# Optimization experiments

Measured on AMD Instinct MI355X. Metric: run time of the kernel, lower is better.

Reference implementation:

```python
import jax, jax.numpy as jnp
import numpy as np

B, T, I, H = 64, 512, 1024, 2048


def setup_inputs() -> dict:
    key = jax.random.key(0)
    ks = jax.random.split(key, 6)
    s = 1.0 / np.sqrt(H).astype(np.float32)
    return {
        "input": jax.random.normal(ks[0], (B, T, I), jnp.float32),
        "internal": jax.random.normal(ks[1], (B, T), jnp.float32) * 0.1,
        "w_ih": jax.random.uniform(ks[2], (H, I), jnp.float32, -s, s),
        "w_hh": jax.random.uniform(ks[3], (H, H), jnp.float32, -s, s),
        "b_ih": jax.random.uniform(ks[4], (H,), jnp.float32, -s, s),
        "b_hh": jax.random.uniform(ks[5], (H,), jnp.float32, -s, s),
        "h0": jnp.zeros((1, B, H), jnp.float32),
        "trunc": 64,
    }


def reference(input, internal, w_ih, w_hh, b_ih, b_hh, h0, trunc):
    # input: [B, T, I]; internal: [B, T] scalar-per-step drive; h0: [1, B, H]
    Tlen = input.shape[1]
    # Hoist the input projection out of the recurrence (same math, one big GEMM).
    x_proj = jnp.einsum('bti,hi->bth', input, w_ih) + b_ih  # [B, T, H]
    # Truncated-BPTT boundaries: state is detached when i % trunc == 0.
    detach_mask = (jnp.arange(Tlen) % trunc) == 0  # [T] bool

    def step(h, xs):
        xp, noise, m = xs  # xp: [B, H], noise: [B], m: scalar bool
        # detach state at truncation boundary (no-op in forward pass)
        h = jnp.where(m, jax.lax.stop_gradient(h), h)
        h_new = jnp.tanh(xp + noise[:, None] + h @ w_hh.T + b_hh)
        return h_new, h_new

    h_last, outs = jax.lax.scan(
        step, h0[0], (x_proj.transpose(1, 0, 2), internal.T, detach_mask))
    # outputs: [B, T, H], final state: [1, B, H]
    return outs.transpose(1, 0, 2), h_last[None]
```

## Files before the change

kernel.cpp:

```cpp
#include <hip/hip_runtime.h>
#include <hip/hip_bf16.h>
#include <math.h>

#define Bb 64
#define Tt 512
#define Ii 1024
#define Hh 2048
#define NBLK 128

typedef __attribute__((ext_vector_type(8))) short bf16x8;
typedef __attribute__((ext_vector_type(8))) unsigned short ushort8;
typedef __attribute__((ext_vector_type(4))) float f32x4;

__device__ __forceinline__ unsigned short f2bf(float x) {
    unsigned int u = __float_as_uint(x);
    unsigned int r = u + 0x7fffu + ((u >> 16) & 1u);
    return (unsigned short)(r >> 16);
}

__global__ __launch_bounds__(256) void cvt_kernel(
    const float* __restrict__ src, unsigned short* __restrict__ dst)
{
    const int i = (blockIdx.x * 256 + threadIdx.x) * 4;
    float4 v = *(const float4*)(src + i);
    ushort4 o;
    o.x = f2bf(v.x); o.y = f2bf(v.y); o.z = f2bf(v.z); o.w = f2bf(v.w);
    *(ushort4*)(dst + i) = o;
}

__global__ __launch_bounds__(512) void init_flags(unsigned int* flags) {
    flags[threadIdx.x] = 0u;
}

__global__ __launch_bounds__(256, 2) void xproj_kernel(
    const float* __restrict__ A,
    const unsigned short* __restrict__ Wbf,
    const float* __restrict__ bias,
    float* __restrict__ out)
{
    __shared__ unsigned short As[128 * 40];
    __shared__ unsigned short Bs[128 * 40];

    const int tid  = threadIdx.x;
    const int lane = tid & 63;
    const int wid  = tid >> 6;
    const int wm   = wid & 1;
    const int wn   = wid >> 1;
    const int rlo  = lane & 15;
    const int khi  = lane >> 4;

    const int m0 = blockIdx.y * 128;
    const int n0 = blockIdx.x * 128;

    f32x4 acc[4][4];
    #pragma unroll
    for (int i = 0; i < 4; ++i)
        #pragma unroll
        for (int j = 0; j < 4; ++j) acc[i][j] = (f32x4)0.f;

    for (int k0 = 0; k0 < Ii; k0 += 32) {
        #pragma unroll
        for (int p = 0; p < 4; ++p) {
            const int flat = p * 256 + tid;
            const int row  = flat >> 3;
            const int c4   = flat & 7;
            float4 v = *(const float4*)(A + (size_t)(m0 + row) * Ii + k0 + c4 * 4);
            ushort4 o;
            o.x = f2bf(v.x); o.y = f2bf(v.y); o.z = f2bf(v.z); o.w = f2bf(v.w);
            *(ushort4*)(As + row * 40 + c4 * 4) = o;
        }
        #pragma unroll
        for (int p = 0; p < 2; ++p) {
            const int flat = p * 256 + tid;
            const int row  = flat >> 2;
            const int c8   = flat & 3;
            ushort8 v = *(const ushort8*)(Wbf + (size_t)(n0 + row) * Ii + k0 + c8 * 8);
            *(ushort8*)(Bs + row * 40 + c8 * 8) = v;
        }
        __syncthreads();

        bf16x8 af[4], bfr[4];
        #pragma unroll
        for (int i = 0; i < 4; ++i)
            af[i] = *(const bf16x8*)(As + (wm * 64 + i * 16 + rlo) * 40 + khi * 8);
        #pragma unroll
        for (int j = 0; j < 4; ++j)
            bfr[j] = *(const bf16x8*)(Bs + (wn * 64 + j * 16 + rlo) * 40 + khi * 8);
        #pragma unroll
        for (int i = 0; i < 4; ++i)
            #pragma unroll
            for (int j = 0; j < 4; ++j)
                acc[i][j] = __builtin_amdgcn_mfma_f32_16x16x32_bf16(
                    af[i], bfr[j], acc[i][j], 0, 0, 0);
        __syncthreads();
    }

    #pragma unroll
    for (int j = 0; j < 4; ++j) {
        const int col = n0 + wn * 64 + j * 16 + rlo;
        const float bj = bias[col];
        #pragma unroll
        for (int i = 0; i < 4; ++i) {
            #pragma unroll
            for (int r = 0; r < 4; ++r) {
                const int m = m0 + wm * 64 + i * 16 + khi * 4 + r;
                out[(size_t)m * Hh + col] = acc[i][j][r] + bj;
            }
        }
    }
}

#define LD_FRAG(dst, base, OFF)                                               \
    asm volatile("global_load_dwordx4 %0, %1, off offset:" OFF " sc0 sc1"     \
                 : "=v"(dst) : "v"(base))

#define LD_FRAG_C(dst, base, OFF)                                             \
    asm volatile("global_load_dwordx4 %0, %1, off offset:" OFF                \
                 : "=v"(dst) : "v"(base))

#define DRAIN16(a)                                                            \
    asm volatile("s_waitcnt vmcnt(0)"                                         \
                 : "+v"(a[0][0]), "+v"(a[0][1]), "+v"(a[0][2]), "+v"(a[0][3]),\
                   "+v"(a[0][4]), "+v"(a[0][5]), "+v"(a[0][6]), "+v"(a[0][7]),\
                   "+v"(a[1][0]), "+v"(a[1][1]), "+v"(a[1][2]), "+v"(a[1][3]),\
                   "+v"(a[1][4]), "+v"(a[1][5]), "+v"(a[1][6]), "+v"(a[1][7]) \
                 :: "memory");                                                \
    __builtin_amdgcn_sched_barrier(0)

#define RAW_BARRIER()                                                         \
    asm volatile("s_waitcnt lgkmcnt(0)\n\ts_barrier" ::: "memory")

__global__ __launch_bounds__(512, 2) void rnn_persistent(
    const unsigned short* __restrict__ w_bf,
    unsigned short* __restrict__ h_bf,
    const float* __restrict__ b_hh,
    const float* __restrict__ internal,
    float* __restrict__ out,
    unsigned int* __restrict__ flags)
{
    __shared__ f32x4 red4[2][8 * 256];

    const int tid  = threadIdx.x;
    const int lane = tid & 63;
    const int wid  = tid >> 6;
    const int rlo  = lane & 15;
    const int khi  = lane >> 4;
    const int blk  = blockIdx.x;
    const int rh   = blk & 1;
    const int cg   = blk >> 1;

    bf16x8 wf[2][8];
    {
        const unsigned short* w0 =
            w_bf + (size_t)(cg * 32 + rlo) * Hh + wid * 256 + khi * 8;
        const unsigned short* w1 = w0 + (size_t)16 * Hh;
        LD_FRAG_C(wf[0][0], w0, "0");   LD_FRAG_C(wf[0][1], w0, "64");
        LD_FRAG_C(wf[0][2], w0, "128"); LD_FRAG_C(wf[0][3], w0, "192");
        LD_FRAG_C(wf[0][4], w0, "256"); LD_FRAG_C(wf[0][5], w0, "320");
        LD_FRAG_C(wf[0][6], w0, "384"); LD_FRAG_C(wf[0][7], w0, "448");
        LD_FRAG_C(wf[1][0], w1, "0");   LD_FRAG_C(wf[1][1], w1, "64");
        LD_FRAG_C(wf[1][2], w1, "128"); LD_FRAG_C(wf[1][3], w1, "192");
        LD_FRAG_C(wf[1][4], w1, "256"); LD_FRAG_C(wf[1][5], w1, "320");
        LD_FRAG_C(wf[1][6], w1, "384"); LD_FRAG_C(wf[1][7], w1, "448");
        DRAIN16(wf);
    }

    const int em    = (tid >> 6) & 1;
    const int ent   = (tid >> 7) & 1;
    const int odd   = lane & 1;
    const int clloc = (ent * 16 + rlo) & ~1;
    const int cl    = cg * 32 + clloc;
    const int rAl   = em * 16 + khi * 4 + 2 * odd;
    const int rAg   = rh * 32 + rAl;
    const int rBg   = rAg + 1;
    const float2 bh2 = (tid < 256) ? *(const float2*)(b_hh + cl)
                                   : make_float2(0.f, 0.f);

    float2 xpA = make_float2(0.f, 0.f), xpB = make_float2(0.f, 0.f);
    float  nzA = 0.f, nzB = 0.f;
    if (tid < 256) {
        xpA = *(const float2*)(out + ((size_t)rAg * Tt + 0) * Hh + cl);
        xpB = *(const float2*)(out + ((size_t)rBg * Tt + 0) * Hh + cl);
        nzA = internal[rAg * Tt + 0];
        nzB = internal[rBg * Tt + 0];
    }
    float2 gA_d = make_float2(0.f, 0.f), gB_d = make_float2(0.f, 0.f);

    unsigned int*       myflag = flags + rh * 256 + cg * 4 + wid;
    const unsigned int* pollf  = flags + rh * 256 + wid * 32 + (lane & 31);

    for (int t = 0; t < Tt; ++t) {
        const bool last = (t == Tt - 1);
        const unsigned short* h_cur = h_bf + (size_t)(t & 1) * Bb * Hh;
        unsigned short*       h_nxt = h_bf + (size_t)((t + 1) & 1) * Bb * Hh;

        if (t) {
            const unsigned int tgt = (unsigned int)t;
            while (true) {
                unsigned int f = __hip_atomic_load(
                    pollf, __ATOMIC_RELAXED, __HIP_MEMORY_SCOPE_AGENT);
                if (__all(f >= tgt)) break;
                __builtin_amdgcn_s_sleep(1);
            }
        }

        const unsigned short* am0 =
            h_cur + (size_t)(rh * 32 + rlo) * Hh + wid * 256 + khi * 8;
        const unsigned short* am1 = am0 + (size_t)16 * Hh;

        bf16x8 a[2][8];
        LD_FRAG(a[0][0], am0, "0");   LD_FRAG(a[0][1], am0, "64");
        LD_FRAG(a[0][2], am0, "128"); LD_FRAG(a[0][3], am0, "192");
        LD_FRAG(a[0][4], am0, "256"); LD_FRAG(a[0][5], am0, "320");
        LD_FRAG(a[0][6], am0, "384"); LD_FRAG(a[0][7], am0, "448");
        LD_FRAG(a[1][0], am1, "0");   LD_FRAG(a[1][1], am1, "64");
        LD_FRAG(a[1][2], am1, "128"); LD_FRAG(a[1][3], am1, "192");
        LD_FRAG(a[1][4], am1, "256"); LD_FRAG(a[1][5], am1, "320");
        LD_FRAG(a[1][6], am1, "384"); LD_FRAG(a[1][7], am1, "448");

        if (tid < 256 && t > 0) {
            *(float2*)(out + ((size_t)rAg * Tt + (t - 1)) * Hh + cl) = gA_d;
            *(float2*)(out + ((size_t)rBg * Tt + (t - 1)) * Hh + cl) = gB_d;
        }

        DRAIN16(a);

        f32x4 acc[2][2];
        #pragma unroll
        for (int m = 0; m < 2; ++m)
            #pragma unroll
            for (int nt = 0; nt < 2; ++nt) acc[m][nt] = (f32x4)0.f;
        #pragma unroll
        for (int kk = 0; kk < 8; ++kk)
            #pragma unroll
            for (int m = 0; m < 2; ++m)
                #pragma unroll
                for (int nt = 0; nt < 2; ++nt)
                    acc[m][nt] = __builtin_amdgcn_mfma_f32_16x16x32_bf16(
                        a[m][kk], wf[nt][kk], acc[m][nt], 0, 0, 0);

        f32x4* rb = red4[t & 1];
        #pragma unroll
        for (int nt = 0; nt < 2; ++nt)
            #pragma unroll
            for (int m = 0; m < 2; ++m)
                rb[wid * 256 + (nt * 2 + m) * 64 + lane] = acc[m][nt];
        RAW_BARRIER();

        if (tid < 256) {
            f32x4 s4 = (f32x4)0.f;
            #pragma unroll
            for (int ks = 0; ks < 8; ++ks)
                s4 += rb[ks * 256 + tid];

            f32x4 o4;
            #pragma unroll
            for (int i = 0; i < 4; ++i)
                o4[i] = __shfl_xor(s4[i], 1, 64);

            const float sA_lo = odd ? o4[2] : s4[0];
            const float sA_hi = odd ? s4[2] : o4[0];
            const float sB_lo = odd ? o4[3] : s4[1];
            const float sB_hi = odd ? s4[3] : o4[1];

            float2 gA, gB;
            gA.x = tanhf(xpA.x + nzA + bh2.x + sA_lo);
            gA.y = tanhf(xpA.y + nzA + bh2.y + sA_hi);
            gB.x = tanhf(xpB.x + nzB + bh2.x + sB_lo);
            gB.y = tanhf(xpB.y + nzB + bh2.y + sB_hi);

            const unsigned int hpA =
                (unsigned int)f2bf(gA.x) | ((unsigned int)f2bf(gA.y) << 16);
            const unsigned int hpB =
                (unsigned int)f2bf(gB.x) | ((unsigned int)f2bf(gB.y) << 16);
            __hip_atomic_store((unsigned int*)h_nxt + ((size_t)rAg * Hh + cl) / 2,
                               hpA, __ATOMIC_RELAXED, __HIP_MEMORY_SCOPE_AGENT);
            __hip_atomic_store((unsigned int*)h_nxt + ((size_t)rBg * Hh + cl) / 2,
                               hpB, __ATOMIC_RELAXED, __HIP_MEMORY_SCOPE_AGENT);

            if (last) {
                *(float2*)(out + ((size_t)rAg * Tt + t) * Hh + cl) = gA;
                *(float2*)(out + ((size_t)rBg * Tt + t) * Hh + cl) = gB;
                float* tail = out + (size_t)Bb * Tt * Hh;
                *(float2*)(tail + (size_t)rAg * Hh + cl) = gA;
                *(float2*)(tail + (size_t)rBg * Hh + cl) = gB;
            } else {
                gA_d = gA; gB_d = gB;

                asm volatile("s_waitcnt vmcnt(0)" ::: "memory");
                if (lane == 0)
                    __hip_atomic_store(myflag, (unsigned int)(t + 1),
                                       __ATOMIC_RELAXED,
                                       __HIP_MEMORY_SCOPE_AGENT);

                xpA = *(const float2*)(out + ((size_t)rAg * Tt + t + 1) * Hh + cl);
                xpB = *(const float2*)(out + ((size_t)rBg * Tt + t + 1) * Hh + cl);
                nzA = internal[rAg * Tt + t + 1];
                nzB = internal[rBg * Tt + t + 1];
            }
        }
    }
}

extern "C" void kernel_launch(void* const* d_in, const int* in_sizes, int n_in,
                              void* d_out, int out_size, void* d_ws, size_t ws_size,
                              hipStream_t stream) {
    const float* input    = (const float*)d_in[0];
    const float* internal = (const float*)d_in[1];
    const float* w_ih     = (const float*)d_in[2];
    const float* w_hh     = (const float*)d_in[3];
    const float* b_ih     = (const float*)d_in[4];
    const float* b_hh     = (const float*)d_in[5];
    const float* h0       = (const float*)d_in[6];
    float* out = (float*)d_out;

    unsigned short* w_hh_bf = (unsigned short*)d_ws;
    unsigned short* w_ih_bf = w_hh_bf + (size_t)Hh * Hh;
    unsigned short* h_bf    = w_ih_bf + (size_t)Hh * Ii;
    unsigned int*   flags   = (unsigned int*)(h_bf + (size_t)2 * Bb * Hh);

    hipLaunchKernelGGL(init_flags, dim3(1), dim3(512), 0, stream, flags);
    hipLaunchKernelGGL(cvt_kernel, dim3((Hh * Hh) / 1024), dim3(256), 0, stream,
                       w_hh, w_hh_bf);
    hipLaunchKernelGGL(cvt_kernel, dim3((Hh * Ii) / 1024), dim3(256), 0, stream,
                       w_ih, w_ih_bf);
    hipLaunchKernelGGL(cvt_kernel, dim3((Bb * Hh) / 1024), dim3(256), 0, stream,
                       h0, h_bf);

    dim3 g1(Hh / 128, (Bb * Tt) / 128);
    hipLaunchKernelGGL(xproj_kernel, g1, dim3(256), 0, stream,
                       input, w_ih_bf, b_ih, out);

    void* args[] = {(void*)&w_hh_bf, (void*)&h_bf, (void*)&b_hh,
                    (void*)&internal, (void*)&out, (void*)&flags};
    hipLaunchCooperativeKernel((void*)rnn_persistent, dim3(NBLK), dim3(512),
                               args, 0, stream);
}
```

Measured before the change: 4.002 ms.

## Halve persistent RNN grid and interleave two batch-half phases per block

```diff
diff --git a/kernel.cpp b/kernel.cpp
--- a/kernel.cpp
+++ b/kernel.cpp
@@ -6,7 +6,7 @@
 #define Tt 512
 #define Ii 1024
 #define Hh 2048
-#define NBLK 128
+#define NBLK 64
 
 typedef __attribute__((ext_vector_type(8))) short bf16x8;
 typedef __attribute__((ext_vector_type(8))) unsigned short ushort8;
@@ -26,6 +26,19 @@
     ushort4 o;
     o.x = f2bf(v.x); o.y = f2bf(v.y); o.z = f2bf(v.z); o.w = f2bf(v.w);
     *(ushort4*)(dst + i) = o;
+}
+
+__global__ __launch_bounds__(256) void cvt_h0(
+    const float* __restrict__ h0, unsigned short* __restrict__ hb)
+{
+    const int idx = (blockIdx.x * 256 + threadIdx.x) * 4;
+    const int b   = idx >> 11;
+    const int col = idx & 2047;
+    float4 v = *(const float4*)(h0 + idx);
+    ushort4 o;
+    o.x = f2bf(v.x); o.y = f2bf(v.y); o.z = f2bf(v.z); o.w = f2bf(v.w);
+    const int ph = b >> 5, r = b & 31;
+    *(ushort4*)(hb + (size_t)(ph * 64 + r) * Hh + col) = o;
 }
 
 __global__ __launch_bounds__(512) void init_flags(unsigned int* flags) {
@@ -145,9 +158,7 @@
     const int wid  = tid >> 6;
     const int rlo  = lane & 15;
     const int khi  = lane >> 4;
-    const int blk  = blockIdx.x;
-    const int rh   = blk & 1;
-    const int cg   = blk >> 1;
+    const int cg   = blockIdx.x;
 
     bf16x8 wf[2][8];
     {
@@ -171,132 +182,148 @@
     const int clloc = (ent * 16 + rlo) & ~1;
     const int cl    = cg * 32 + clloc;
     const int rAl   = em * 16 + khi * 4 + 2 * odd;
-    const int rAg   = rh * 32 + rAl;
-    const int rBg   = rAg + 1;
     const float2 bh2 = (tid < 256) ? *(const float2*)(b_hh + cl)
                                    : make_float2(0.f, 0.f);
 
-    float2 xpA = make_float2(0.f, 0.f), xpB = make_float2(0.f, 0.f);
-    float  nzA = 0.f, nzB = 0.f;
+    float2 xpA[2], xpB[2], gAd[2], gBd[2];
+    float  nzA[2], nzB[2];
+    #pragma unroll
+    for (int ph = 0; ph < 2; ++ph) {
+        xpA[ph] = make_float2(0.f, 0.f); xpB[ph] = make_float2(0.f, 0.f);
+        gAd[ph] = make_float2(0.f, 0.f); gBd[ph] = make_float2(0.f, 0.f);
+        nzA[ph] = 0.f; nzB[ph] = 0.f;
+    }
     if (tid < 256) {
-        xpA = *(const float2*)(out + ((size_t)rAg * Tt + 0) * Hh + cl);
-        xpB = *(const float2*)(out + ((size_t)rBg * Tt + 0) * Hh + cl);
-        nzA = internal[rAg * Tt + 0];
-        nzB = internal[rBg * Tt + 0];
-    }
-    float2 gA_d = make_float2(0.f, 0.f), gB_d = make_float2(0.f, 0.f);
-
-    unsigned int*       myflag = flags + rh * 256 + cg * 4 + wid;
-    const unsigned int* pollf  = flags + rh * 256 + wid * 32 + (lane & 31);
+        #pragma unroll
+        for (int ph = 0; ph < 2; ++ph) {
+            const int rA = ph * 32 + rAl, rB = rA + 1;
+            xpA[ph] = *(const float2*)(out + ((size_t)rA * Tt + 0) * Hh + cl);
+            xpB[ph] = *(const float2*)(out + ((size_t)rB * Tt + 0) * Hh + cl);
+            nzA[ph] = internal[rA * Tt + 0];
+            nzB[ph] = internal[rB * Tt + 0];
+        }
+    }
 
     for (int t = 0; t < Tt; ++t) {
         const bool last = (t == Tt - 1);
-        const unsigned short* h_cur = h_bf + (size_t)(t & 1) * Bb * Hh;
-        unsigned short*       h_nxt = h_bf + (size_t)((t + 1) & 1) * Bb * Hh;
-
-        if (t) {
-            const unsigned int tgt = (unsigned int)t;
-            while (true) {
-                unsigned int f = __hip_atomic_load(
-                    pollf, __ATOMIC_RELAXED, __HIP_MEMORY_SCOPE_AGENT);
-                if (__all(f >= tgt)) break;
-                __builtin_amdgcn_s_sleep(1);
+        #pragma unroll
+        for (int ph = 0; ph < 2; ++ph) {
+            const unsigned short* h_cur =
+                h_bf + (size_t)(ph * 64 + (t & 1) * 32) * Hh;
+            unsigned short* h_nxt =
+                h_bf + (size_t)(ph * 64 + ((t + 1) & 1) * 32) * Hh;
+
+            if (t) {
+                const unsigned int tgt = (unsigned int)t;
+                const unsigned int* pf =
+                    flags + ph * 256 + wid * 32 + (lane & 31);
+                while (true) {
+                    unsigned int f = __hip_atomic_load(
+                        pf, __ATOMIC_RELAXED, __HIP_MEMORY_SCOPE_AGENT);
+                    if (__all(f >= tgt)) break;
+                    __builtin_amdgcn_s_sleep(1);
+                }
             }
-        }
-
-        const unsigned short* am0 =
-            h_cur + (size_t)(rh * 32 + rlo) * Hh + wid * 256 + khi * 8;
-        const unsigned short* am1 = am0 + (size_t)16 * Hh;
-
-        bf16x8 a[2][8];
-        LD_FRAG(a[0][0], am0, "0");   LD_FRAG(a[0][1], am0, "64");
-        LD_FRAG(a[0][2], am0, "128"); LD_FRAG(a[0][3], am0, "192");
-        LD_FRAG(a[0][4], am0, "256"); LD_FRAG(a[0][5], am0, "320");
-        LD_FRAG(a[0][6], am0, "384"); LD_FRAG(a[0][7], am0, "448");
-        LD_FRAG(a[1][0], am1, "0");   LD_FRAG(a[1][1], am1, "64");
-        LD_FRAG(a[1][2], am1, "128"); LD_FRAG(a[1][3], am1, "192");
-        LD_FRAG(a[1][4], am1, "256"); LD_FRAG(a[1][5], am1, "320");
-        LD_FRAG(a[1][6], am1, "384"); LD_FRAG(a[1][7], am1, "448");
-
-        if (tid < 256 && t > 0) {
-            *(float2*)(out + ((size_t)rAg * Tt + (t - 1)) * Hh + cl) = gA_d;
-            *(float2*)(out + ((size_t)rBg * Tt + (t - 1)) * Hh + cl) = gB_d;
-        }
-
-        DRAIN16(a);
-
-        f32x4 acc[2][2];
-        #pragma unroll
-        for (int m = 0; m < 2; ++m)
-            #pragma unroll
-            for (int nt = 0; nt < 2; ++nt) acc[m][nt] = (f32x4)0.f;
-        #pragma unroll
-        for (int kk = 0; kk < 8; ++kk)
+
+            const unsigned short* am0 =
+                h_cur + (size_t)rlo * Hh + wid * 256 + khi * 8;
+            const unsigned short* am1 = am0 + (size_t)16 * Hh;
+
+            bf16x8 a[2][8];
+            LD_FRAG(a[0][0], am0, "0");   LD_FRAG(a[0][1], am0, "64");
+            LD_FRAG(a[0][2], am0, "128"); LD_FRAG(a[0][3], am0, "192");
+            LD_FRAG(a[0][4], am0, "256"); LD_FRAG(a[0][5], am0, "320");
+            LD_FRAG(a[0][6], am0, "384"); LD_FRAG(a[0][7], am0, "448");
+            LD_FRAG(a[1][0], am1, "0");   LD_FRAG(a[1][1], am1, "64");
+            LD_FRAG(a[1][2], am1, "128"); LD_FRAG(a[1][3], am1, "192");
+            LD_FRAG(a[1][4], am1, "256"); LD_FRAG(a[1][5], am1, "320");
+            LD_FRAG(a[1][6], am1, "384"); LD_FRAG(a[1][7], am1, "448");
+
+            if (tid < 256 && t > 0) {
+                const int rA = ph * 32 + rAl, rB = rA + 1;
+                *(float2*)(out + ((size_t)rA * Tt + (t - 1)) * Hh + cl) = gAd[ph];
+                *(float2*)(out + ((size_t)rB * Tt + (t - 1)) * Hh + cl) = gBd[ph];
+            }
+
+            DRAIN16(a);
+
+            f32x4 acc[2][2];
             #pragma unroll
             for (int m = 0; m < 2; ++m)
                 #pragma unroll
-                for (int nt = 0; nt < 2; ++nt)
-                    acc[m][nt] = __builtin_amdgcn_mfma_f32_16x16x32_bf16(
-                        a[m][kk], wf[nt][kk], acc[m][nt], 0, 0, 0);
-
-        f32x4* rb = red4[t & 1];
-        #pragma unroll
-        for (int nt = 0; nt < 2; ++nt)
-            #pragma unroll
-            for (int m = 0; m < 2; ++m)
-                rb[wid * 256 + (nt * 2 + m) * 64 + lane] = acc[m][nt];
-        RAW_BARRIER();
-
-        if (tid < 256) {
-            f32x4 s4 = (f32x4)0.f;
-            #pragma unroll
-            for (int ks = 0; ks < 8; ++ks)
-                s4 += rb[ks * 256 + tid];
-
-            f32x4 o4;
-            #pragma unroll
-            for (int i = 0; i < 4; ++i)
-                o4[i] = __shfl_xor(s4[i], 1, 64);
-
-            const float sA_lo = odd ? o4[2] : s4[0];
-            const float sA_hi = odd ? s4[2] : o4[0];
-            const float sB_lo = odd ? o4[3] : s4[1];
-            const float sB_hi = odd ? s4[3] : o4[1];
-
-            float2 gA, gB;
-            gA.x = tanhf(xpA.x + nzA + bh2.x + sA_lo);
-            gA.y = tanhf(xpA.y + nzA + bh2.y + sA_hi);
-            gB.x = tanhf(xpB.x + nzB + bh2.x + sB_lo);
-            gB.y = tanhf(xpB.y + nzB + bh2.y + sB_hi);
-
-            const unsigned int hpA =
-                (unsigned int)f2bf(gA.x) | ((unsigned int)f2bf(gA.y) << 16);
-            const unsigned int hpB =
-                (unsigned int)f2bf(gB.x) | ((unsigned int)f2bf(gB.y) << 16);
-            __hip_atomic_store((unsigned int*)h_nxt + ((size_t)rAg * Hh + cl) / 2,
-                               hpA, __ATOMIC_RELAXED, __HIP_MEMORY_SCOPE_AGENT);
-            __hip_atomic_store((unsigned int*)h_nxt + ((size_t)rBg * Hh + cl) / 2,
-                               hpB, __ATOMIC_RELAXED, __HIP_MEMORY_SCOPE_AGENT);
-
-            if (last) {
-                *(float2*)(out + ((size_t)rAg * Tt + t) * Hh + cl) = gA;
-                *(float2*)(out + ((size_t)rBg * Tt + t) * Hh + cl) = gB;
-                float* tail = out + (size_t)Bb * Tt * Hh;
-                *(float2*)(tail + (size_t)rAg * Hh + cl) = gA;
-                *(float2*)(tail + (size_t)rBg * Hh + cl) = gB;
-            } else {
-                gA_d = gA; gB_d = gB;
-
-                asm volatile("s_waitcnt vmcnt(0)" ::: "memory");
-                if (lane == 0)
-                    __hip_atomic_store(myflag, (unsigned int)(t + 1),
-                                       __ATOMIC_RELAXED,
-                                       __HIP_MEMORY_SCOPE_AGENT);
-
-                xpA = *(const float2*)(out + ((size_t)rAg * Tt + t + 1) * Hh + cl);
-                xpB = *(const float2*)(out + ((size_t)rBg * Tt + t + 1) * Hh + cl);
-                nzA = internal[rAg * Tt + t + 1];
-                nzB = internal[rBg * Tt + t + 1];
+                for (int nt = 0; nt < 2; ++nt) acc[m][nt] = (f32x4)0.f;
+            #pragma unroll
+            for (int kk = 0; kk < 8; ++kk)
+                #pragma unroll
+                for (int m = 0; m < 2; ++m)
+                    #pragma unroll
+                    for (int nt = 0; nt < 2; ++nt)
+                        acc[m][nt] = __builtin_amdgcn_mfma_f32_16x16x32_bf16(
+                            a[m][kk], wf[nt][kk], acc[m][nt], 0, 0, 0);
+
+            f32x4* rb = red4[ph];
+            #pragma unroll
+            for (int nt = 0; nt < 2; ++nt)
+                #pragma unroll
+                for (int m = 0; m < 2; ++m)
+                    rb[wid * 256 + (nt * 2 + m) * 64 + lane] = acc[m][nt];
+            RAW_BARRIER();
+
+            if (tid < 256) {
+                f32x4 s4 = (f32x4)0.f;
+                #pragma unroll
+                for (int ks = 0; ks < 8; ++ks)
+                    s4 += rb[ks * 256 + tid];
+
+                f32x4 o4;
+                #pragma unroll
+                for (int i = 0; i < 4; ++i)
+                    o4[i] = __shfl_xor(s4[i], 1, 64);
+
+                const float sA_lo = odd ? o4[2] : s4[0];
+                const float sA_hi = odd ? s4[2] : o4[0];
+                const float sB_lo = odd ? o4[3] : s4[1];
+                const float sB_hi = odd ? s4[3] : o4[1];
+
+                float2 gA, gB;
+                gA.x = tanhf(xpA[ph].x + nzA[ph] + bh2.x + sA_lo);
+                gA.y = tanhf(xpA[ph].y + nzA[ph] + bh2.y + sA_hi);
+                gB.x = tanhf(xpB[ph].x + nzB[ph] + bh2.x + sB_lo);
+                gB.y = tanhf(xpB[ph].y + nzB[ph] + bh2.y + sB_hi);
+
+                const int rA = ph * 32 + rAl, rB = rA + 1;
+                const unsigned int hpA =
+                    (unsigned int)f2bf(gA.x) | ((unsigned int)f2bf(gA.y) << 16);
+                const unsigned int hpB =
+                    (unsigned int)f2bf(gB.x) | ((unsigned int)f2bf(gB.y) << 16);
+                __hip_atomic_store(
+                    (unsigned int*)h_nxt + ((size_t)rAl * Hh + cl) / 2,
+                    hpA, __ATOMIC_RELAXED, __HIP_MEMORY_SCOPE_AGENT);
+                __hip_atomic_store(
+                    (unsigned int*)h_nxt + ((size_t)(rAl + 1) * Hh + cl) / 2,
+                    hpB, __ATOMIC_RELAXED, __HIP_MEMORY_SCOPE_AGENT);
+
+                if (last) {
+                    *(float2*)(out + ((size_t)rA * Tt + t) * Hh + cl) = gA;
+                    *(float2*)(out + ((size_t)rB * Tt + t) * Hh + cl) = gB;
+                    float* tail = out + (size_t)Bb * Tt * Hh;
+                    *(float2*)(tail + (size_t)rA * Hh + cl) = gA;
+                    *(float2*)(tail + (size_t)rB * Hh + cl) = gB;
+                } else {
+                    gAd[ph] = gA; gBd[ph] = gB;
+
+                    asm volatile("s_waitcnt vmcnt(0)" ::: "memory");
+                    if (lane == 0)
+                        __hip_atomic_store(flags + ph * 256 + cg * 4 + wid,
+                                           (unsigned int)(t + 1),
+                                           __ATOMIC_RELAXED,
+                                           __HIP_MEMORY_SCOPE_AGENT);
+
+                    xpA[ph] = *(const float2*)(out + ((size_t)rA * Tt + t + 1) * Hh + cl);
+                    xpB[ph] = *(const float2*)(out + ((size_t)rB * Tt + t + 1) * Hh + cl);
+                    nzA[ph] = internal[rA * Tt + t + 1];
+                    nzB[ph] = internal[rB * Tt + t + 1];
+                }
             }
         }
     }
@@ -324,7 +351,7 @@
                        w_hh, w_hh_bf);
     hipLaunchKernelGGL(cvt_kernel, dim3((Hh * Ii) / 1024), dim3(256), 0, stream,
                        w_ih, w_ih_bf);
-    hipLaunchKernelGGL(cvt_kernel, dim3((Bb * Hh) / 1024), dim3(256), 0, stream,
+    hipLaunchKernelGGL(cvt_h0, dim3((Bb * Hh) / 1024), dim3(256), 0, stream,
                        h0, h_bf);
 
     dim3 g1(Hh / 128, (Bb * Tt) / 128);
```

Result: slower. 5.511 ms (+37.7%).
